# Performance work log

Measured on AMD Instinct MI355X. Metric: run time of the kernel, lower is better.

Reference implementation:

```python
import jax, jax.numpy as jnp
import numpy as np
import math

D = 1024
H = 16
B = 4
N = 2048


def setup_inputs() -> dict:
    key = jax.random.key(0)
    ks = jax.random.split(key, 10)
    scale_qkv = 0.01
    def kaiming_uniform(k, shape, scale):
        # attenuated_kaiming_uniform_: fan_in = shape[1], gain for leaky_relu a=sqrt(5)
        fan_in = shape[1]
        gain = math.sqrt(2.0 / (1 + 5.0))
        bound = math.sqrt(3.0) * gain * scale / math.sqrt(fan_in)
        return jax.random.uniform(k, shape, jnp.float32, -bound, bound)
    return {
        "x_q": jax.random.normal(ks[0], (B, N, D), jnp.float32),
        "x_kv": jax.random.normal(ks[1], (B, N, D), jnp.float32),
        "Wq": kaiming_uniform(ks[2], (D, D), scale_qkv),
        "bq": jnp.zeros((D,), jnp.float32),
        "Wk": kaiming_uniform(ks[3], (D, D), scale_qkv),
        "bk": jnp.zeros((D,), jnp.float32),
        "Wv": kaiming_uniform(ks[4], (D, D), scale_qkv),
        "bv": jnp.zeros((D,), jnp.float32),
        "Wo": kaiming_uniform(ks[5], (D, D), 1.0),
        "bo": jnp.zeros((D,), jnp.float32),
    }


def reference(x_q, x_kv, Wq, bq, Wk, bk, Wv, bv, Wo, bo):
    bs, n, d = x_q.shape
    hd = d // H  # head dim
    # torch Linear: y = x @ W^T + b
    q = x_q @ Wq.T + bq
    k = x_kv @ Wk.T + bk
    v = x_kv @ Wv.T + bv
    # reshape to [bs, H, n, hd]
    q = q.reshape(bs, n, H, hd).transpose(0, 2, 1, 3)
    k = k.reshape(bs, n, H, hd).transpose(0, 2, 1, 3)
    v = v.reshape(bs, n, H, hd).transpose(0, 2, 1, 3)
    scores = jnp.einsum("bhqd,bhkd->bhqk", q, k) / math.sqrt(hd)
    seq_ids = jnp.arange(n)
    causal = (seq_ids[None, :] <= seq_ids[:, None]).astype(scores.dtype)  # [n, n]
    scores = scores + (1.0 - causal) * -10000.0
    probs = jax.nn.softmax(scores, axis=-1)
    out = jnp.einsum("bhqk,bhkd->bhqd", probs, v)
    out = out.transpose(0, 2, 1, 3).reshape(bs, n, d)
    return out @ Wo.T + bo
```

## Files before the change

### kernel.cpp

```cpp
#include <hip/hip_runtime.h>

typedef unsigned short u16;
typedef unsigned int u32;
typedef __attribute__((ext_vector_type(8))) short short8;
typedef __attribute__((ext_vector_type(4))) float f32x4;
typedef __attribute__((ext_vector_type(16))) float f32x16;
typedef __attribute__((ext_vector_type(4))) unsigned u32x4;

#define ASYNC_CP16(gsrc, ldst) \
  __builtin_amdgcn_global_load_lds((__attribute__((address_space(1))) void*)(gsrc), \
                                   (__attribute__((address_space(3))) void*)(ldst), 16, 0, 0)

static __device__ __forceinline__ u16 f2bf(float f) {
  u32 u = __builtin_bit_cast(u32, f);
  u = u + 0x7fffu + ((u >> 16) & 1u);
  return (u16)(u >> 16);
}
static __device__ __forceinline__ u32 pk2(float a, float b) {
  return (u32)f2bf(a) | ((u32)f2bf(b) << 16);
}
static __device__ __forceinline__ u32 cvtpk(float lo, float hi) {
  u32 r;
  asm("v_cvt_pk_bf16_f32 %0, %1, %2" : "=v"(r) : "v"(lo), "v"(hi));
  return r;
}
static __device__ __forceinline__ void plswap(u32 &a, u32 &b) {
  asm("v_permlane32_swap_b32 %0, %1" : "+v"(a), "+v"(b));
}

__global__ __launch_bounds__(256) void convert_all(
    const float* __restrict__ xq, const float* __restrict__ xkv,
    const float* __restrict__ wq, const float* __restrict__ wk,
    const float* __restrict__ wv, const float* __restrict__ wo,
    u16* __restrict__ dst)
{
  long i = ((long)blockIdx.x * 256 + threadIdx.x) * 4;
  const float* s; long o;
  if      (i < 8388608)  { s = xq;  o = i; }
  else if (i < 16777216) { s = xkv; o = i - 8388608; }
  else if (i < 17825792) { s = wq;  o = i - 16777216; }
  else if (i < 18874368) { s = wk;  o = i - 17825792; }
  else if (i < 19922944) { s = wv;  o = i - 18874368; }
  else                   { s = wo;  o = i - 19922944; }
  float4 v = *(const float4*)(s + o);
  uint2 pkv; pkv.x = pk2(v.x, v.y); pkv.y = pk2(v.z, v.w);
  *(uint2*)(dst + i) = pkv;
}

template<int EPI>
__global__ __launch_bounds__(512, 2)
void gemm8(const u16* __restrict__ Axq, const u16* __restrict__ Axkv,
           const u16* __restrict__ W0, const u16* __restrict__ W1, const u16* __restrict__ W2,
           const float* __restrict__ b0, const float* __restrict__ b1, const float* __restrict__ b2,
           u16* __restrict__ Qo, u16* __restrict__ Ko, u16* __restrict__ Vo,
           float* __restrict__ Fo)
{
  __shared__ u16 lds[65536];
  const int tid = threadIdx.x;
  const int w = tid >> 6, lane = tid & 63;
  const int wm = w >> 2, wn = w & 3;
  const int bm = blockIdx.x, bn = blockIdx.y, z = blockIdx.z;
  const int l15 = lane & 15, l4 = lane >> 4;

  const u16* A; const u16* W; const float* bias;
  if (EPI == 0) {
    A    = (z == 0) ? Axq : Axkv;
    W    = (z == 0) ? W0 : (z == 1) ? W1 : W2;
    bias = (z == 0) ? b0 : (z == 1) ? b1 : b2;
  } else {
    A = Axq; W = W0; bias = b0;
  }
  const u16* Ag = A + (long)bm*256*1024;
  const u16* Wg = W + (long)bn*256*1024;

  int srco[2][2], dsto[2][2];
#pragma unroll
  for (int h = 0; h < 2; ++h)
#pragma unroll
    for (int c = 0; c < 2; ++c) {
      const int rowl = (c*512 + tid) >> 3;
      const int kch  = (tid & 7) ^ (rowl & 7);
      srco[h][c] = (h*128 + rowl)*1024 + kch*8;
      dsto[h][c] = h*8192 + c*4096 + tid*8;
    }

  f32x4 acc[8][4];
#pragma unroll
  for (int i = 0; i < 8; ++i)
#pragma unroll
    for (int j = 0; j < 4; ++j)
      acc[i][j] = (f32x4){0.f,0.f,0.f,0.f};

#pragma unroll
  for (int h = 0; h < 2; ++h)
#pragma unroll
    for (int c = 0; c < 2; ++c) {
      ASYNC_CP16(Ag + srco[h][c], &lds[dsto[h][c]]);
      ASYNC_CP16(Wg + srco[h][c], &lds[32768 + dsto[h][c]]);
    }
  asm volatile("s_waitcnt vmcnt(0)" ::: "memory");
  __builtin_amdgcn_s_barrier();

  const int sx0 = ((l4)     ^ (l15 & 7)) * 8;
  const int sx1 = ((4 + l4) ^ (l15 & 7)) * 8;

  for (int t = 0; t < 16; ++t) {
    const int cur = t & 1;
    const u16* la = &lds[cur*16384];
    const u16* lb = &lds[32768 + cur*16384];

    if (t < 15) {
      const int k0 = (t + 1)*64;
      u16* da = &lds[(cur^1)*16384];
      u16* db = &lds[32768 + (cur^1)*16384];
#pragma unroll
      for (int h = 0; h < 2; ++h)
#pragma unroll
        for (int c = 0; c < 2; ++c) {
          ASYNC_CP16(Ag + srco[h][c] + k0, da + dsto[h][c]);
          ASYNC_CP16(Wg + srco[h][c] + k0, db + dsto[h][c]);
        }
    }
    short8 bfr[4][2];
#pragma unroll
    for (int fn = 0; fn < 4; ++fn) {
      const u16* rb = lb + (wn*64 + fn*16 + l15)*64;
      bfr[fn][0] = *(const short8*)(rb + sx0);
      bfr[fn][1] = *(const short8*)(rb + sx1);
    }

#pragma unroll
    for (int q = 0; q < 4; ++q) {
      short8 af[2][2];
#pragma unroll
      for (int i = 0; i < 2; ++i) {
        const u16* ra = la + (wm*128 + (q*2 + i)*16 + l15)*64;
        af[i][0] = *(const short8*)(ra + sx0);
        af[i][1] = *(const short8*)(ra + sx1);
      }
      __builtin_amdgcn_s_barrier();
      asm volatile("s_waitcnt lgkmcnt(0)" ::: "memory");
      __builtin_amdgcn_sched_barrier(0);
      __builtin_amdgcn_s_setprio(1);
#pragma unroll
      for (int i = 0; i < 2; ++i)
#pragma unroll
        for (int fn = 0; fn < 4; ++fn) {
          acc[q*2+i][fn] = __builtin_amdgcn_mfma_f32_16x16x32_bf16(af[i][0], bfr[fn][0], acc[q*2+i][fn], 0, 0, 0);
          acc[q*2+i][fn] = __builtin_amdgcn_mfma_f32_16x16x32_bf16(af[i][1], bfr[fn][1], acc[q*2+i][fn], 0, 0, 0);
        }
      __builtin_amdgcn_s_setprio(0);
      __builtin_amdgcn_sched_barrier(0);
      if (q == 3 && t < 15)
        asm volatile("s_waitcnt vmcnt(0)" ::: "memory");
      __builtin_amdgcn_s_barrier();
    }
  }

#pragma unroll
  for (int fn = 0; fn < 4; ++fn) {
    const int colg = bn*256 + wn*64 + fn*16 + l15;
    const float bb = bias[colg];
#pragma unroll
    for (int fm = 0; fm < 8; ++fm) {
      const int rowg = bm*256 + wm*128 + fm*16 + l4*4;
      if (EPI == 1) {
#pragma unroll
        for (int r = 0; r < 4; ++r)
          Fo[(long)(rowg + r)*1024 + colg] = acc[fm][fn][r] + bb;
      } else {
        const int b  = rowg >> 11, n0 = rowg & 2047;
        const int h  = colg >> 6,  c  = colg & 63;
        const int bh = b*16 + h;
        const long hb = (long)bh*131072 + (long)(n0 >> 7)*8192;
        if (z == 0) {
#pragma unroll
          for (int r = 0; r < 4; ++r)
            Qo[((long)bh*2048 + n0 + r)*64 + c] = f2bf((acc[fm][fn][r] + bb) * 0.18033688f);
        } else if (z == 1) {
          const long base = hb + (long)(c >> 3)*1024 + (n0 & 127)*8 + (c & 7);
#pragma unroll
          for (int r = 0; r < 4; ++r)
            Ko[base + r*8] = f2bf(acc[fm][fn][r] + bb);
        } else {
          const long base = hb + (long)((n0 & 127) >> 3)*512 + (long)c*8 + (n0 & 7);
          uint2 pkv;
          pkv.x = pk2(acc[fm][fn][0] + bb, acc[fm][fn][1] + bb);
          pkv.y = pk2(acc[fm][fn][2] + bb, acc[fm][fn][3] + bb);
          *(uint2*)(Vo + base) = pkv;
        }
      }
    }
  }
}

__global__ __launch_bounds__(512, 4)
void attn_k(const u16* __restrict__ Q, const u16* __restrict__ K,
            const u16* __restrict__ V, u16* __restrict__ AO)
{
  __shared__ u16 lk[2][8192];
  __shared__ u16 lv[2][8192];
  const int tid = threadIdx.x;
  const int w = tid >> 6, lane = tid & 63;
  const int l31 = lane & 31, l5 = lane >> 5;
  const int wq = w & 3, hh = w >> 2;
  const int qt = (gridDim.x - 1) - blockIdx.x;
  const int bh = blockIdx.y;
  const int q0 = qt*128;
  const int qg = q0 + wq*32 + l31;
  const u16* Qh = Q + (long)bh*131072;
  const u16* Kh = K + (long)bh*131072;
  const u16* Vh = V + (long)bh*131072;

  short8 qf[4];
#pragma unroll
  for (int ks = 0; ks < 4; ++ks)
    qf[ks] = *(const short8*)&Qh[(long)qg*64 + ks*16 + l5*8];

  f32x16 o0 = (f32x16)0.0f;
  f32x16 o1 = (f32x16)0.0f;
  float rsum = 0.f;

  const int koff = l5*2048 + l31*16;
  const int voff = l5*1024 + l31*16;
  const int ktmax = qt;

#pragma unroll
  for (int c = 0; c < 2; ++c) {
    int tp = c*512 + tid;
    ASYNC_CP16(Kh + tp*8, &lk[0][tp*8]);
    ASYNC_CP16(Vh + tp*8, &lv[0][tp*8]);
  }

  for (int kt = 0; kt <= ktmax; ++kt) {
    const int cur = kt & 1;
    if (kt < ktmax) {
      const long off = (long)(kt + 1)*8192;
#pragma unroll
      for (int c = 0; c < 2; ++c) {
        int tp = c*512 + tid;
        ASYNC_CP16(Kh + off + tp*8, &lk[cur^1][tp*8]);
        ASYNC_CP16(Vh + off + tp*8, &lv[cur^1][tp*8]);
      }
      asm volatile("s_waitcnt vmcnt(4)" ::: "memory");
    } else {
      asm volatile("s_waitcnt vmcnt(0)" ::: "memory");
    }
    __builtin_amdgcn_s_barrier();

    const char* lkc = (const char*)lk + cur*16384;
    const char* lvc = (const char*)lv + cur*16384;

    const bool active = !(kt == ktmax && hh*64 > wq*32 + 31);
    if (active) {
      short8 pf[4];
#pragma unroll
      for (int sbl = 0; sbl < 2; ++sbl) {
        f32x16 sa = (f32x16)0.0f;
#pragma unroll
        for (int ks = 0; ks < 4; ++ks) {
          short8 kf = *(const short8*)(lkc + koff + ks*4096 + (hh*2 + sbl)*512);
          sa = __builtin_amdgcn_mfma_f32_32x32x16_bf16(kf, qf[ks], sa, 0, 0, 0);
        }
        if (kt == ktmax) {
          const int kb = kt*128 + hh*64 + sbl*32 + 4*l5;
#pragma unroll
          for (int g = 0; g < 4; ++g)
#pragma unroll
            for (int rr = 0; rr < 4; ++rr)
              if (kb + 8*g + rr > qg) sa[4*g + rr] = -1e30f;
        }
        float p[16];
#pragma unroll
        for (int r = 0; r < 16; ++r) p[r] = __builtin_amdgcn_exp2f(sa[r]);
#pragma unroll
        for (int g = 0; g < 4; ++g)
          rsum += (p[4*g] + p[4*g+1]) + (p[4*g+2] + p[4*g+3]);
        u32 cc[4][2];
#pragma unroll
        for (int g = 0; g < 4; ++g) {
          cc[g][0] = cvtpk(p[4*g],   p[4*g+1]);
          cc[g][1] = cvtpk(p[4*g+2], p[4*g+3]);
        }
        plswap(cc[0][0], cc[1][0]); plswap(cc[0][1], cc[1][1]);
        plswap(cc[2][0], cc[3][0]); plswap(cc[2][1], cc[3][1]);
        u32x4 pw0 = {cc[0][0], cc[0][1], cc[1][0], cc[1][1]};
        u32x4 pw1 = {cc[2][0], cc[2][1], cc[3][0], cc[3][1]};
        pf[sbl*2]     = __builtin_bit_cast(short8, pw0);
        pf[sbl*2 + 1] = __builtin_bit_cast(short8, pw1);
      }
#pragma unroll
      for (int j = 0; j < 4; ++j) {
        const char* vb = lvc + voff + (hh*4 + j)*2048;
        short8 vf0 = *(const short8*)(vb);
        o0 = __builtin_amdgcn_mfma_f32_32x32x16_bf16(vf0, pf[j], o0, 0, 0, 0);
        short8 vf1 = *(const short8*)(vb + 512);
        o1 = __builtin_amdgcn_mfma_f32_32x32x16_bf16(vf1, pf[j], o1, 0, 0, 0);
      }
    }

    asm volatile("" ::: "memory");
    __builtin_amdgcn_s_barrier();
  }

  __syncthreads();
  float* exf = (float*)&lk[0][0];
  float* rxf = (float*)&lv[0][0];
  const int sw = lane & 7;
  float* xb = exf + wq*2048 + lane*32;

  if (hh == 1) {
#pragma unroll
    for (int c = 0; c < 4; ++c) {
      f32x4 v; v[0]=o0[c*4]; v[1]=o0[c*4+1]; v[2]=o0[c*4+2]; v[3]=o0[c*4+3];
      *(f32x4*)(xb + ((c ^ sw)*4)) = v;
    }
#pragma unroll
    for (int c = 0; c < 4; ++c) {
      f32x4 v; v[0]=o1[c*4]; v[1]=o1[c*4+1]; v[2]=o1[c*4+2]; v[3]=o1[c*4+3];
      *(f32x4*)(xb + (((c+4) ^ sw)*4)) = v;
    }
    rxf[wq*64 + lane] = rsum;
  }
  __syncthreads();
  if (hh == 0) {
    float rt = rsum + rxf[wq*64 + lane];
    rt += __shfl_xor(rt, 32, 64);
    const float inv = 1.0f / rt;
#pragma unroll
    for (int c = 0; c < 4; ++c) {
      f32x4 v = *(const f32x4*)(xb + ((c ^ sw)*4));
      o0[c*4] += v[0]; o0[c*4+1] += v[1]; o0[c*4+2] += v[2]; o0[c*4+3] += v[3];
    }
#pragma unroll
    for (int c = 0; c < 4; ++c) {
      f32x4 v = *(const f32x4*)(xb + (((c+4) ^ sw)*4));
      o1[c*4] += v[0]; o1[c*4+1] += v[1]; o1[c*4+2] += v[2]; o1[c*4+3] += v[3];
    }
    const int b = bh >> 4, h = bh & 15;
    const long tok = (long)b*2048 + qg;
    u16* dst = AO + tok*1024 + h*64;
#pragma unroll
    for (int g = 0; g < 4; ++g) {
      uint2 pkv;
      pkv.x = pk2(o0[4*g]*inv,   o0[4*g+1]*inv);
      pkv.y = pk2(o0[4*g+2]*inv, o0[4*g+3]*inv);
      *(uint2*)(dst + 8*g + 4*l5) = pkv;
    }
#pragma unroll
    for (int g = 0; g < 4; ++g) {
      uint2 pkv;
      pkv.x = pk2(o1[4*g]*inv,   o1[4*g+1]*inv);
      pkv.y = pk2(o1[4*g+2]*inv, o1[4*g+3]*inv);
      *(uint2*)(dst + 32 + 8*g + 4*l5) = pkv;
    }
  }
}

extern "C" void kernel_launch(void* const* d_in, const int* in_sizes, int n_in,
                              void* d_out, int out_size, void* d_ws, size_t ws_size,
                              hipStream_t stream)
{
  const float* xq  = (const float*)d_in[0];
  const float* xkv = (const float*)d_in[1];
  const float* Wq  = (const float*)d_in[2];
  const float* bq  = (const float*)d_in[3];
  const float* Wk  = (const float*)d_in[4];
  const float* bk  = (const float*)d_in[5];
  const float* Wv  = (const float*)d_in[6];
  const float* bv  = (const float*)d_in[7];
  const float* Wo  = (const float*)d_in[8];
  const float* bo  = (const float*)d_in[9];

  u16* ws    = (u16*)d_ws;
  u16* xq_b  = ws;
  u16* xkv_b = xq_b  + (1l<<23);
  u16* wq_b  = xkv_b + (1l<<23);
  u16* wk_b  = wq_b  + (1l<<20);
  u16* wv_b  = wk_b  + (1l<<20);
  u16* wo_b  = wv_b  + (1l<<20);
  u16* Qb    = wo_b  + (1l<<20);
  u16* Kb    = Qb    + (1l<<23);
  u16* Vb    = Kb    + (1l<<23);
  u16* Ab    = Vb    + (1l<<23);

  convert_all<<<20480, 256, 0, stream>>>(xq, xkv, Wq, Wk, Wv, Wo, ws);
  gemm8<0><<<dim3(32,4,3), 512, 0, stream>>>(xq_b, xkv_b, wq_b, wk_b, wv_b,
                                             bq, bk, bv, Qb, Kb, Vb, nullptr);
  attn_k<<<dim3(16,64), 512, 0, stream>>>(Qb, Kb, Vb, Ab);
  gemm8<1><<<dim3(32,4,1), 512, 0, stream>>>(Ab, nullptr, wo_b, nullptr, nullptr,
                                             bo, nullptr, nullptr,
                                             nullptr, nullptr, nullptr,
                                             (float*)d_out);
}
```

Measured before the change: 310.8 us.

## Prefetch two K-tiles ahead in QKV GEMM and add smaller-tile output projection kernel

The QKV GEMM now issues its async global-to-LDS loads two k-steps ahead, placing each new load after the last MFMA group of a step. It waits with vmcnt(8) rather than vmcnt(0), so global latency overlaps more compute. The output projection moves from the 256x256-tile gemm8 (only 128 blocks on the device) to a new 128x128-tile, 256-thread kernel with 512 blocks, which should fill more compute units. The new kernel uses an unswizzled LDS layout and a shorter K step, which may cause bank conflicts and more barrier overhead.

```diff
diff --git a/kernel.cpp b/kernel.cpp
--- a/kernel.cpp
+++ b/kernel.cpp
@@ -47,13 +47,11 @@
   *(uint2*)(dst + i) = pkv;
 }
 
-template<int EPI>
 __global__ __launch_bounds__(512, 2)
 void gemm8(const u16* __restrict__ Axq, const u16* __restrict__ Axkv,
            const u16* __restrict__ W0, const u16* __restrict__ W1, const u16* __restrict__ W2,
            const float* __restrict__ b0, const float* __restrict__ b1, const float* __restrict__ b2,
-           u16* __restrict__ Qo, u16* __restrict__ Ko, u16* __restrict__ Vo,
-           float* __restrict__ Fo)
+           u16* __restrict__ Qo, u16* __restrict__ Ko, u16* __restrict__ Vo)
 {
   __shared__ u16 lds[65536];
   const int tid = threadIdx.x;
@@ -62,14 +60,9 @@
   const int bm = blockIdx.x, bn = blockIdx.y, z = blockIdx.z;
   const int l15 = lane & 15, l4 = lane >> 4;
 
-  const u16* A; const u16* W; const float* bias;
-  if (EPI == 0) {
-    A    = (z == 0) ? Axq : Axkv;
-    W    = (z == 0) ? W0 : (z == 1) ? W1 : W2;
-    bias = (z == 0) ? b0 : (z == 1) ? b1 : b2;
-  } else {
-    A = Axq; W = W0; bias = b0;
-  }
+  const u16* A    = (z == 0) ? Axq : Axkv;
+  const u16* W    = (z == 0) ? W0 : (z == 1) ? W1 : W2;
+  const float* bias = (z == 0) ? b0 : (z == 1) ? b1 : b2;
   const u16* Ag = A + (long)bm*256*1024;
   const u16* Wg = W + (long)bn*256*1024;
 
@@ -98,7 +91,14 @@
       ASYNC_CP16(Ag + srco[h][c], &lds[dsto[h][c]]);
       ASYNC_CP16(Wg + srco[h][c], &lds[32768 + dsto[h][c]]);
     }
-  asm volatile("s_waitcnt vmcnt(0)" ::: "memory");
+#pragma unroll
+  for (int h = 0; h < 2; ++h)
+#pragma unroll
+    for (int c = 0; c < 2; ++c) {
+      ASYNC_CP16(Ag + srco[h][c] + 64, &lds[16384 + dsto[h][c]]);
+      ASYNC_CP16(Wg + srco[h][c] + 64, &lds[49152 + dsto[h][c]]);
+    }
+  asm volatile("s_waitcnt vmcnt(8)" ::: "memory");
   __builtin_amdgcn_s_barrier();
 
   const int sx0 = ((l4)     ^ (l15 & 7)) * 8;
@@ -109,18 +109,6 @@
     const u16* la = &lds[cur*16384];
     const u16* lb = &lds[32768 + cur*16384];
 
-    if (t < 15) {
-      const int k0 = (t + 1)*64;
-      u16* da = &lds[(cur^1)*16384];
-      u16* db = &lds[32768 + (cur^1)*16384];
-#pragma unroll
-      for (int h = 0; h < 2; ++h)
-#pragma unroll
-        for (int c = 0; c < 2; ++c) {
-          ASYNC_CP16(Ag + srco[h][c] + k0, da + dsto[h][c]);
-          ASYNC_CP16(Wg + srco[h][c] + k0, db + dsto[h][c]);
-        }
-    }
     short8 bfr[4][2];
 #pragma unroll
     for (int fn = 0; fn < 4; ++fn) {
@@ -138,9 +126,9 @@
         af[i][0] = *(const short8*)(ra + sx0);
         af[i][1] = *(const short8*)(ra + sx1);
       }
-      __builtin_amdgcn_s_barrier();
       asm volatile("s_waitcnt lgkmcnt(0)" ::: "memory");
       __builtin_amdgcn_sched_barrier(0);
+      __builtin_amdgcn_s_barrier();
       __builtin_amdgcn_s_setprio(1);
 #pragma unroll
       for (int i = 0; i < 2; ++i)
@@ -151,8 +139,23 @@
         }
       __builtin_amdgcn_s_setprio(0);
       __builtin_amdgcn_sched_barrier(0);
-      if (q == 3 && t < 15)
-        asm volatile("s_waitcnt vmcnt(0)" ::: "memory");
+      if (q == 3) {
+        if (t <= 13) {
+          const int k0 = (t + 2)*64;
+          u16* da = &lds[cur*16384];
+          u16* db = &lds[32768 + cur*16384];
+#pragma unroll
+          for (int h = 0; h < 2; ++h)
+#pragma unroll
+            for (int c = 0; c < 2; ++c) {
+              ASYNC_CP16(Ag + srco[h][c] + k0, da + dsto[h][c]);
+              ASYNC_CP16(Wg + srco[h][c] + k0, db + dsto[h][c]);
+            }
+          asm volatile("s_waitcnt vmcnt(8)" ::: "memory");
+        } else if (t == 14) {
+          asm volatile("s_waitcnt vmcnt(0)" ::: "memory");
+        }
+      }
       __builtin_amdgcn_s_barrier();
     }
   }
@@ -164,32 +167,104 @@
 #pragma unroll
     for (int fm = 0; fm < 8; ++fm) {
       const int rowg = bm*256 + wm*128 + fm*16 + l4*4;
-      if (EPI == 1) {
+      const int b  = rowg >> 11, n0 = rowg & 2047;
+      const int h  = colg >> 6,  c  = colg & 63;
+      const int bh = b*16 + h;
+      const long hb = (long)bh*131072 + (long)(n0 >> 7)*8192;
+      if (z == 0) {
 #pragma unroll
         for (int r = 0; r < 4; ++r)
-          Fo[(long)(rowg + r)*1024 + colg] = acc[fm][fn][r] + bb;
+          Qo[((long)bh*2048 + n0 + r)*64 + c] = f2bf((acc[fm][fn][r] + bb) * 0.18033688f);
+      } else if (z == 1) {
+        const long base = hb + (long)(c >> 3)*1024 + (n0 & 127)*8 + (c & 7);
+#pragma unroll
+        for (int r = 0; r < 4; ++r)
+          Ko[base + r*8] = f2bf(acc[fm][fn][r] + bb);
       } else {
-        const int b  = rowg >> 11, n0 = rowg & 2047;
-        const int h  = colg >> 6,  c  = colg & 63;
-        const int bh = b*16 + h;
-        const long hb = (long)bh*131072 + (long)(n0 >> 7)*8192;
-        if (z == 0) {
-#pragma unroll
-          for (int r = 0; r < 4; ++r)
-            Qo[((long)bh*2048 + n0 + r)*64 + c] = f2bf((acc[fm][fn][r] + bb) * 0.18033688f);
-        } else if (z == 1) {
-          const long base = hb + (long)(c >> 3)*1024 + (n0 & 127)*8 + (c & 7);
-#pragma unroll
-          for (int r = 0; r < 4; ++r)
-            Ko[base + r*8] = f2bf(acc[fm][fn][r] + bb);
-        } else {
-          const long base = hb + (long)((n0 & 127) >> 3)*512 + (long)c*8 + (n0 & 7);
-          uint2 pkv;
-          pkv.x = pk2(acc[fm][fn][0] + bb, acc[fm][fn][1] + bb);
-          pkv.y = pk2(acc[fm][fn][2] + bb, acc[fm][fn][3] + bb);
-          *(uint2*)(Vo + base) = pkv;
-        }
-      }
+        const long base = hb + (long)((n0 & 127) >> 3)*512 + (long)c*8 + (n0 & 7);
+        uint2 pkv;
+        pkv.x = pk2(acc[fm][fn][0] + bb, acc[fm][fn][1] + bb);
+        pkv.y = pk2(acc[fm][fn][2] + bb, acc[fm][fn][3] + bb);
+        *(uint2*)(Vo + base) = pkv;
+      }
+    }
+  }
+}
+
+__global__ __launch_bounds__(256)
+void gemm_o(const u16* __restrict__ A, const u16* __restrict__ W,
+            const float* __restrict__ bias, float* __restrict__ Fo)
+{
+  __shared__ u16 lsa[2][128*32];
+  __shared__ u16 lsb[2][128*32];
+  const int tid = threadIdx.x;
+  const int w = tid >> 6, lane = tid & 63;
+  const int wr = w >> 1, wc = w & 1;
+  const int bm = blockIdx.x, bn = blockIdx.y;
+  const int l15 = lane & 15, l4 = lane >> 4;
+
+  const u16* Ag = A + (long)bm*128*1024;
+  const u16* Wg = W + (long)bn*128*1024;
+
+  f32x4 acc[4][4];
+#pragma unroll
+  for (int i = 0; i < 4; ++i)
+#pragma unroll
+    for (int j = 0; j < 4; ++j)
+      acc[i][j] = (f32x4){0.f,0.f,0.f,0.f};
+
+#pragma unroll
+  for (int c = 0; c < 2; ++c) {
+    int tp = c*256 + tid;
+    int row = tp >> 2, col = (tp & 3) * 8;
+    ASYNC_CP16(Ag + (long)row*1024 + col, &lsa[0][tp*8]);
+    ASYNC_CP16(Wg + (long)row*1024 + col, &lsb[0][tp*8]);
+  }
+
+  for (int t = 0; t < 32; ++t) {
+    const int cur = t & 1;
+    if (t < 31) {
+      const int k0 = (t + 1) * 32;
+#pragma unroll
+      for (int c = 0; c < 2; ++c) {
+        int tp = c*256 + tid;
+        int row = tp >> 2, col = (tp & 3) * 8;
+        ASYNC_CP16(Ag + (long)row*1024 + k0 + col, &lsa[cur^1][tp*8]);
+        ASYNC_CP16(Wg + (long)row*1024 + k0 + col, &lsb[cur^1][tp*8]);
+      }
+      asm volatile("s_waitcnt vmcnt(4)" ::: "memory");
+    } else {
+      asm volatile("s_waitcnt vmcnt(0)" ::: "memory");
+    }
+    __builtin_amdgcn_s_barrier();
+
+    short8 af[4], bfr[4];
+#pragma unroll
+    for (int i = 0; i < 4; ++i)
+      af[i] = *(const short8*)&lsa[cur][(wr*64 + i*16 + l15)*32 + l4*8];
+#pragma unroll
+    for (int j = 0; j < 4; ++j)
+      bfr[j] = *(const short8*)&lsb[cur][(wc*64 + j*16 + l15)*32 + l4*8];
+#pragma unroll
+    for (int i = 0; i < 4; ++i)
+#pragma unroll
+      for (int j = 0; j < 4; ++j)
+        acc[i][j] = __builtin_amdgcn_mfma_f32_16x16x32_bf16(af[i], bfr[j], acc[i][j], 0, 0, 0);
+
+    asm volatile("" ::: "memory");
+    __builtin_amdgcn_s_barrier();
+  }
+
+#pragma unroll
+  for (int j = 0; j < 4; ++j) {
+    const int colg = bn*128 + wc*64 + j*16 + l15;
+    const float bb = bias[colg];
+#pragma unroll
+    for (int i = 0; i < 4; ++i) {
+      const int rowg = bm*128 + wr*64 + i*16 + l4*4;
+#pragma unroll
+      for (int r = 0; r < 4; ++r)
+        Fo[(long)(rowg + r)*1024 + colg] = acc[i][j][r] + bb;
     }
   }
 }
@@ -385,11 +460,8 @@
   u16* Ab    = Vb    + (1l<<23);
 
   convert_all<<<20480, 256, 0, stream>>>(xq, xkv, Wq, Wk, Wv, Wo, ws);
-  gemm8<0><<<dim3(32,4,3), 512, 0, stream>>>(xq_b, xkv_b, wq_b, wk_b, wv_b,
-                                             bq, bk, bv, Qb, Kb, Vb, nullptr);
+  gemm8<<<dim3(32,4,3), 512, 0, stream>>>(xq_b, xkv_b, wq_b, wk_b, wv_b,
+                                          bq, bk, bv, Qb, Kb, Vb);
   attn_k<<<dim3(16,64), 512, 0, stream>>>(Qb, Kb, Vb, Ab);
-  gemm8<1><<<dim3(32,4,1), 512, 0, stream>>>(Ab, nullptr, wo_b, nullptr, nullptr,
-                                             bo, nullptr, nullptr,
-                                             nullptr, nullptr, nullptr,
-                                             (float*)d_out);
-}
+  gemm_o<<<dim3(64,8), 256, 0, stream>>>(Ab, wo_b, bo, (float*)d_out);
+}
```

New measurement: 313.6 us. No clear change (+0.9%).
